# Performance work log

Hardware: AMD Instinct MI355X
Metric: run time of the kernel (lower is better)

## Reference

```python
import jax, jax.numpy as jnp
import numpy as np

INPUT_DIM = 256
UNITS = 256
BATCH = 65536


def _glorot(key, shape):
    fan_in, fan_out = shape
    limit = np.sqrt(6.0 / (fan_in + fan_out)).astype(np.float32)
    return jax.random.uniform(key, shape, jnp.float32, -limit, limit)


def setup_inputs() -> dict:
    key = jax.random.key(0)
    ks = jax.random.split(key, 8)
    d = {
        "inputs": jax.random.normal(ks[0], (BATCH, INPUT_DIM), jnp.float32),
        "h_prev": jax.random.normal(ks[1], (BATCH, UNITS), jnp.float32),
        "c_prev": jax.random.normal(ks[2], (BATCH, UNITS), jnp.float32),
        "W_f": _glorot(ks[3], (INPUT_DIM + UNITS, UNITS)),
        "W_i": _glorot(ks[4], (INPUT_DIM + UNITS, UNITS)),
        "W_c": _glorot(ks[5], (INPUT_DIM + UNITS, UNITS)),
        "W_o": _glorot(ks[6], (INPUT_DIM + UNITS, UNITS)),
        "b_f": jnp.zeros((UNITS,), jnp.float32),
        "b_i": jnp.zeros((UNITS,), jnp.float32),
        "b_c": jnp.zeros((UNITS,), jnp.float32),
        "b_o": jnp.zeros((UNITS,), jnp.float32),
    }
    return d


def reference(inputs, h_prev, c_prev, W_f, W_i, W_c, W_o, b_f, b_i, b_c, b_o):
    # z: [B, input_dim + units]
    z = jnp.concatenate([inputs, h_prev], axis=-1)
    f = jax.nn.sigmoid(z @ W_f + b_f)
    i = jax.nn.sigmoid(z @ W_i + b_i)
    c_tilde = jnp.tanh(z @ W_c + b_c)
    c = f * c_prev + i * c_tilde
    o = jax.nn.sigmoid(z @ W_o + b_o)
    h = o * jnp.tanh(c)
    return h, c
```

## Files before the change

### kernel.cpp

```cpp
#include <hip/hip_runtime.h>
#include <hip/hip_bf16.h>
#include <stdint.h>

#define BATCH   65536
#define UNITS   256
#define NCH     16
#define ROWP    68
#define GSZ     (64 * ROWP)
#define SMEM_BYTES 40960

using f32x16 = __attribute__((ext_vector_type(16))) float;
using bf16x8 = __attribute__((ext_vector_type(8))) short;

__device__ __forceinline__ short f2bf(float f) {
  union { float f; unsigned u; } v; v.f = f;
  unsigned r = v.u + 0x7FFFu + ((v.u >> 16) & 1u);
  return (short)(r >> 16);
}
__device__ __forceinline__ float bf2f(short s) {
  union { float f; unsigned u; } v; v.u = ((unsigned)(unsigned short)s) << 16;
  return v.f;
}
__device__ __forceinline__ unsigned pk2(float a, float b) {
  union { __hip_bfloat162 h; unsigned u; } cv;
  cv.h = __float22bfloat162_rn(make_float2(a, b));
  return cv.u;
}
__device__ __forceinline__ bf16x8 cvt8(float4 a, float4 b) {
  union { unsigned u[4]; bf16x8 v; } r;
  r.u[0] = pk2(a.x, a.y); r.u[1] = pk2(a.z, a.w);
  r.u[2] = pk2(b.x, b.y); r.u[3] = pk2(b.z, b.w);
  return r.v;
}
#define LOG2E 1.4426950408889634f
__device__ __forceinline__ float fast_sigmoid(float x) {
  return __builtin_amdgcn_rcpf(1.f + __builtin_amdgcn_exp2f(x * -LOG2E));
}
__device__ __forceinline__ float fast_tanh(float x) {
  return 2.f * __builtin_amdgcn_rcpf(1.f + __builtin_amdgcn_exp2f(x * (-2.f * LOG2E))) - 1.f;
}

#define BAR() do { asm volatile("s_waitcnt lgkmcnt(0)" ::: "memory"); \
                   __builtin_amdgcn_s_barrier(); } while (0)
#define WAITV(n) asm volatile("s_waitcnt vmcnt(" #n ")" ::: "memory")

__device__ __forceinline__ void gload_lds16(const void* gsrc, void* ldst) {
  __builtin_amdgcn_global_load_lds(
      (const __attribute__((address_space(1))) void*)gsrc,
      (__attribute__((address_space(3))) void*)ldst,
      16, 0, 0);
}

__global__ void cvt_weights(const float* __restrict__ Wf, const float* __restrict__ Wi,
                            const float* __restrict__ Wc, const float* __restrict__ Wo,
                            short* __restrict__ Wt) {
  int idx = blockIdx.x * 256 + threadIdx.x;
  int g   = idx >> 17;
  int k   = (idx >> 8) & 511;
  int col = idx & 255;
  const float* W = (g == 0) ? Wf : (g == 1) ? Wi : (g == 2) ? Wc : Wo;
  float val = W[k * 256 + col];
  int nb = col >> 6, n = col & 63;
  int kg = k >> 3, k8 = k & 7;
  int out = (((g * 4 + nb) * 64 + kg) * 64 + n) * 8 + k8;
  Wt[out] = f2bf(val);
}

__global__ __launch_bounds__(256, 4) void lstm_fused(
    const float* __restrict__ x, const float* __restrict__ hprev,
    const float* __restrict__ cprev, const short* __restrict__ Wt,
    const float* __restrict__ bfp, const float* __restrict__ bip,
    const float* __restrict__ bcp, const float* __restrict__ bop,
    float* __restrict__ hout, float* __restrict__ cout)
{
  extern __shared__ __align__(16) char smem[];
  const int tid  = threadIdx.x;
  const int g    = tid >> 6;
  const int lane = tid & 63;
  const int la   = lane & 31;
  const int hh   = lane >> 5;

  int bid = blockIdx.x;
  int wg  = (bid & 7) * 512 + (bid >> 3);
  const int m0 = (wg >> 2) * 64;
  const int nb = wg & 3;
  const int n0 = nb * 64;

  const short* WtG = Wt + ((size_t)(g * 4 + nb)) * 32768;

  f32x16 acc[2][2] = {};
  float4 vA[2][2];

  const int arow  = tid >> 2;
  const int q     = tid & 3;
  const int slotW = arow ^ (q << 2);

  char* Abase = smem;
  char* Bbase = smem + 8192;

  auto ldA = [&](int c) {
    const float* base = (c < 8) ? x : hprev;
    const float* rowp = base + (size_t)(m0 + arow) * 256 + (c & 7) * 32 + q * 8;
    vA[c & 1][0] = *(const float4*)(rowp);
    vA[c & 1][1] = *(const float4*)(rowp + 4);
  };
  auto wrA = [&](int c) {
    char* Ab = Abase + (c & 1) * 4096;
    *(bf16x8*)(Ab + q * 1024 + slotW * 16) = cvt8(vA[c & 1][0], vA[c & 1][1]);
  };
  auto stageB = [&](int c) {
    char* ldst = Bbase + (c & 1) * 16384 + g * 4096;
    const short* gs = WtG + c * 2048 + lane * 8;
#pragma unroll
    for (int i = 0; i < 4; ++i)
      gload_lds16(gs + i * 512, ldst + i * 1024);
  };
  auto compute = [&](int c) {
    const char* Ab = Abase + (c & 1) * 4096;
    const char* Bl = Bbase + (c & 1) * 16384 + g * 4096;
#pragma unroll
    for (int ks = 0; ks < 2; ++ks) {
      const int kg = 2 * ks + hh;
      const int ao = kg * 1024 + ((la ^ (kg << 2)) * 16);
      bf16x8 a0 = *(const bf16x8*)(Ab + ao);
      bf16x8 a1 = *(const bf16x8*)(Ab + ao + 512);
      bf16x8 b0 = *(const bf16x8*)(Bl + kg * 1024 + la * 16);
      bf16x8 b1 = *(const bf16x8*)(Bl + kg * 1024 + la * 16 + 512);
      acc[0][0] = __builtin_amdgcn_mfma_f32_32x32x16_bf16(a0, b0, acc[0][0], 0, 0, 0);
      acc[0][1] = __builtin_amdgcn_mfma_f32_32x32x16_bf16(a0, b1, acc[0][1], 0, 0, 0);
      acc[1][0] = __builtin_amdgcn_mfma_f32_32x32x16_bf16(a1, b0, acc[1][0], 0, 0, 0);
      acc[1][1] = __builtin_amdgcn_mfma_f32_32x32x16_bf16(a1, b1, acc[1][1], 0, 0, 0);
    }
  };

  ldA(0); stageB(0); ldA(1); stageB(1);
  wrA(0);

#pragma unroll
  for (int c = 0; c < NCH; ++c) {
    if (c + 2 < NCH) ldA(c + 2);
    if (c < NCH - 2)      WAITV(8);
    else if (c == NCH - 2) WAITV(6);
    else                   WAITV(0);
    BAR();
    if (c + 1 < NCH) wrA(c + 1);
    compute(c);
    __builtin_amdgcn_sched_barrier(0);
    if (c + 2 < NCH) stageB(c + 2);
  }

  const int ccol = tid & 63;
  const int rg   = tid >> 6;
  const size_t gbase = (size_t)(m0 + rg * 16) * 256 + n0 + ccol;
  float cp[16];
#pragma unroll
  for (int j = 0; j < 16; ++j) cp[j] = cprev[gbase + (size_t)j * 256];

  const float* bptr = (g == 0) ? bfp : (g == 1) ? bip : (g == 2) ? bcp : bop;
  const float bias0 = bptr[n0 + la];
  const float bias1 = bptr[n0 + 32 + la];
  BAR();
  short* G = (short*)smem;
#pragma unroll
  for (int mi = 0; mi < 2; ++mi)
#pragma unroll
    for (int ni = 0; ni < 2; ++ni) {
      const float bias = ni ? bias1 : bias0;
      const int   col  = la + ni * 32;
#pragma unroll
      for (int rq = 0; rq < 4; ++rq) {
        const int row0 = rq * 8 + 4 * hh + mi * 32;
        float t[4];
#pragma unroll
        for (int e = 0; e < 4; ++e) {
          float vv = acc[mi][ni][rq * 4 + e] + bias;
          t[e] = (g == 2) ? fast_tanh(vv) : fast_sigmoid(vv);
        }
        uint2 u; u.x = pk2(t[0], t[1]); u.y = pk2(t[2], t[3]);
        *(uint2*)(G + g * GSZ + col * ROWP + row0) = u;
      }
    }
  BAR();

  {
    const short* Gp = G + ccol * ROWP + rg * 16;
    bf16x8 gf[4][2];
#pragma unroll
    for (int gg = 0; gg < 4; ++gg) {
      gf[gg][0] = *(const bf16x8*)(Gp + gg * GSZ);
      gf[gg][1] = *(const bf16x8*)(Gp + gg * GSZ + 8);
    }
#pragma unroll
    for (int j = 0; j < 16; ++j) {
      float fg = bf2f(gf[0][j >> 3][j & 7]);
      float ig = bf2f(gf[1][j >> 3][j & 7]);
      float cg = bf2f(gf[2][j >> 3][j & 7]);
      float og = bf2f(gf[3][j >> 3][j & 7]);
      float cnew = fg * cp[j] + ig * cg;
      float hnew = og * fast_tanh(cnew);
      hout[gbase + (size_t)j * 256] = hnew;
      cout[gbase + (size_t)j * 256] = cnew;
    }
  }
}

extern "C" void kernel_launch(void* const* d_in, const int* in_sizes, int n_in,
                              void* d_out, int out_size, void* d_ws, size_t ws_size,
                              hipStream_t stream) {
  const float* x     = (const float*)d_in[0];
  const float* hprev = (const float*)d_in[1];
  const float* cprev = (const float*)d_in[2];
  const float* Wf    = (const float*)d_in[3];
  const float* Wi    = (const float*)d_in[4];
  const float* Wc    = (const float*)d_in[5];
  const float* Wo    = (const float*)d_in[6];
  const float* bfp   = (const float*)d_in[7];
  const float* bip   = (const float*)d_in[8];
  const float* bcp   = (const float*)d_in[9];
  const float* bop   = (const float*)d_in[10];
  float* out = (float*)d_out;
  short* Wt  = (short*)d_ws;

  cvt_weights<<<2048, 256, 0, stream>>>(Wf, Wi, Wc, Wo, Wt);

  lstm_fused<<<dim3(4096), dim3(256), SMEM_BYTES, stream>>>(
      x, hprev, cprev, Wt, bfp, bip, bcp, bop,
      out, out + (size_t)BATCH * UNITS);
}
```

Baseline: 143.5 us.

## Double block M tile to 128 rows with 512 threads sharing B stages

Each block now handles 128 batch rows using 512 threads (two M halves), so each weight chunk staged into LDS is reused by twice as many rows and global weight traffic is halved. The B buffer becomes triple-buffered, and the A global loads move after compute so they issue next to the B staging, with simplified vmcnt waits. The epilogue writes and combines the gate tiles in two phases through the same LDS region. The cost is more LDS per block (64KB), which may cut resident blocks per CU, plus extra barriers in the epilogue.

```diff
diff --git a/kernel.cpp b/kernel.cpp
--- a/kernel.cpp
+++ b/kernel.cpp
@@ -7,7 +7,7 @@
 #define NCH     16
 #define ROWP    68
 #define GSZ     (64 * ROWP)
-#define SMEM_BYTES 40960
+#define SMEM_BYTES 65536
 
 using f32x16 = __attribute__((ext_vector_type(16))) float;
 using bf16x8 = __attribute__((ext_vector_type(8))) short;
@@ -66,7 +66,7 @@
   Wt[out] = f2bf(val);
 }
 
-__global__ __launch_bounds__(256, 4) void lstm_fused(
+__global__ __launch_bounds__(512, 4) void lstm_fused(
     const float* __restrict__ x, const float* __restrict__ hprev,
     const float* __restrict__ cprev, const short* __restrict__ Wt,
     const float* __restrict__ bfp, const float* __restrict__ bip,
@@ -75,28 +75,28 @@
 {
   extern __shared__ __align__(16) char smem[];
   const int tid  = threadIdx.x;
-  const int g    = tid >> 6;
+  const int gg   = (tid >> 6) & 3;
+  const int mh   = tid >> 8;
   const int lane = tid & 63;
   const int la   = lane & 31;
   const int hh   = lane >> 5;
 
   int bid = blockIdx.x;
-  int wg  = (bid & 7) * 512 + (bid >> 3);
-  const int m0 = (wg >> 2) * 64;
+  int wg  = (bid & 7) * 256 + (bid >> 3);
+  const int m0 = (wg >> 2) * 128;
   const int nb = wg & 3;
   const int n0 = nb * 64;
 
-  const short* WtG = Wt + ((size_t)(g * 4 + nb)) * 32768;
+  const short* WtG = Wt + ((size_t)(gg * 4 + nb)) * 32768;
 
   f32x16 acc[2][2] = {};
   float4 vA[2][2];
 
-  const int arow  = tid >> 2;
-  const int q     = tid & 3;
-  const int slotW = arow ^ (q << 2);
+  const int arow = tid >> 2;
+  const int q    = tid & 3;
 
   char* Abase = smem;
-  char* Bbase = smem + 8192;
+  char* Bbase = smem + 16384;
 
   auto ldA = [&](int c) {
     const float* base = (c < 8) ? x : hprev;
@@ -105,23 +105,22 @@
     vA[c & 1][1] = *(const float4*)(rowp + 4);
   };
   auto wrA = [&](int c) {
-    char* Ab = Abase + (c & 1) * 4096;
-    *(bf16x8*)(Ab + q * 1024 + slotW * 16) = cvt8(vA[c & 1][0], vA[c & 1][1]);
+    char* Ab = Abase + (c & 1) * 8192;
+    *(bf16x8*)(Ab + q * 2048 + (arow ^ (q << 2)) * 16) = cvt8(vA[c & 1][0], vA[c & 1][1]);
   };
   auto stageB = [&](int c) {
-    char* ldst = Bbase + (c & 1) * 16384 + g * 4096;
-    const short* gs = WtG + c * 2048 + lane * 8;
-#pragma unroll
-    for (int i = 0; i < 4; ++i)
-      gload_lds16(gs + i * 512, ldst + i * 1024);
+    char* ldst = Bbase + (c % 3) * 16384 + gg * 4096 + mh * 2048;
+    const short* gs = WtG + c * 2048 + mh * 1024 + lane * 8;
+    gload_lds16(gs, ldst);
+    gload_lds16(gs + 512, ldst + 1024);
   };
   auto compute = [&](int c) {
-    const char* Ab = Abase + (c & 1) * 4096;
-    const char* Bl = Bbase + (c & 1) * 16384 + g * 4096;
+    const char* Ab = Abase + (c & 1) * 8192;
+    const char* Bl = Bbase + (c % 3) * 16384 + gg * 4096;
 #pragma unroll
     for (int ks = 0; ks < 2; ++ks) {
       const int kg = 2 * ks + hh;
-      const int ao = kg * 1024 + ((la ^ (kg << 2)) * 16);
+      const int ao = kg * 2048 + (((mh * 64 + la) ^ (kg << 2)) * 16);
       bf16x8 a0 = *(const bf16x8*)(Ab + ao);
       bf16x8 a1 = *(const bf16x8*)(Ab + ao + 512);
       bf16x8 b0 = *(const bf16x8*)(Bl + kg * 1024 + la * 16);
@@ -138,70 +137,77 @@
 
 #pragma unroll
   for (int c = 0; c < NCH; ++c) {
-    if (c + 2 < NCH) ldA(c + 2);
-    if (c < NCH - 2)      WAITV(8);
-    else if (c == NCH - 2) WAITV(6);
-    else                   WAITV(0);
+    if (c == NCH - 1) { WAITV(0); } else { WAITV(4); }
     BAR();
     if (c + 1 < NCH) wrA(c + 1);
     compute(c);
     __builtin_amdgcn_sched_barrier(0);
-    if (c + 2 < NCH) stageB(c + 2);
+    if (c + 2 < NCH) { ldA(c + 2); stageB(c + 2); }
   }
 
   const int ccol = tid & 63;
-  const int rg   = tid >> 6;
-  const size_t gbase = (size_t)(m0 + rg * 16) * 256 + n0 + ccol;
+  const int rseg = (tid >> 6) & 7;
   float cp[16];
 #pragma unroll
-  for (int j = 0; j < 16; ++j) cp[j] = cprev[gbase + (size_t)j * 256];
-
-  const float* bptr = (g == 0) ? bfp : (g == 1) ? bip : (g == 2) ? bcp : bop;
+  for (int ph = 0; ph < 2; ++ph) {
+    const size_t gb = (size_t)(m0 + ph * 64 + rseg * 8) * 256 + n0 + ccol;
+#pragma unroll
+    for (int j = 0; j < 8; ++j) cp[ph * 8 + j] = cprev[gb + (size_t)j * 256];
+  }
+
+  const float* bptr = (gg == 0) ? bfp : (gg == 1) ? bip : (gg == 2) ? bcp : bop;
   const float bias0 = bptr[n0 + la];
   const float bias1 = bptr[n0 + 32 + la];
-  BAR();
   short* G = (short*)smem;
-#pragma unroll
-  for (int mi = 0; mi < 2; ++mi)
-#pragma unroll
-    for (int ni = 0; ni < 2; ++ni) {
-      const float bias = ni ? bias1 : bias0;
-      const int   col  = la + ni * 32;
-#pragma unroll
-      for (int rq = 0; rq < 4; ++rq) {
-        const int row0 = rq * 8 + 4 * hh + mi * 32;
-        float t[4];
-#pragma unroll
-        for (int e = 0; e < 4; ++e) {
-          float vv = acc[mi][ni][rq * 4 + e] + bias;
-          t[e] = (g == 2) ? fast_tanh(vv) : fast_sigmoid(vv);
+
+  auto writeG = [&]() {
+#pragma unroll
+    for (int mi = 0; mi < 2; ++mi)
+#pragma unroll
+      for (int ni = 0; ni < 2; ++ni) {
+        const float bias = ni ? bias1 : bias0;
+        const int   col  = la + ni * 32;
+#pragma unroll
+        for (int rq = 0; rq < 4; ++rq) {
+          const int row0 = rq * 8 + 4 * hh + mi * 32;
+          float t[4];
+#pragma unroll
+          for (int e = 0; e < 4; ++e) {
+            float vv = acc[mi][ni][rq * 4 + e] + bias;
+            t[e] = (gg == 2) ? fast_tanh(vv) : fast_sigmoid(vv);
+          }
+          uint2 u; u.x = pk2(t[0], t[1]); u.y = pk2(t[2], t[3]);
+          *(uint2*)(G + gg * GSZ + col * ROWP + row0) = u;
         }
-        uint2 u; u.x = pk2(t[0], t[1]); u.y = pk2(t[2], t[3]);
-        *(uint2*)(G + g * GSZ + col * ROWP + row0) = u;
       }
+  };
+  auto combine = [&](int ph) {
+    const short* Gp = G + ccol * ROWP + rseg * 8;
+    bf16x8 gf[4];
+#pragma unroll
+    for (int t = 0; t < 4; ++t) gf[t] = *(const bf16x8*)(Gp + t * GSZ);
+    const size_t gb = (size_t)(m0 + ph * 64 + rseg * 8) * 256 + n0 + ccol;
+#pragma unroll
+    for (int j = 0; j < 8; ++j) {
+      float fg = bf2f(gf[0][j]);
+      float ig = bf2f(gf[1][j]);
+      float cg = bf2f(gf[2][j]);
+      float og = bf2f(gf[3][j]);
+      float cnew = fg * cp[ph * 8 + j] + ig * cg;
+      float hnew = og * fast_tanh(cnew);
+      hout[gb + (size_t)j * 256] = hnew;
+      cout[gb + (size_t)j * 256] = cnew;
     }
-  BAR();
-
-  {
-    const short* Gp = G + ccol * ROWP + rg * 16;
-    bf16x8 gf[4][2];
-#pragma unroll
-    for (int gg = 0; gg < 4; ++gg) {
-      gf[gg][0] = *(const bf16x8*)(Gp + gg * GSZ);
-      gf[gg][1] = *(const bf16x8*)(Gp + gg * GSZ + 8);
-    }
-#pragma unroll
-    for (int j = 0; j < 16; ++j) {
-      float fg = bf2f(gf[0][j >> 3][j & 7]);
-      float ig = bf2f(gf[1][j >> 3][j & 7]);
-      float cg = bf2f(gf[2][j >> 3][j & 7]);
-      float og = bf2f(gf[3][j >> 3][j & 7]);
-      float cnew = fg * cp[j] + ig * cg;
-      float hnew = og * fast_tanh(cnew);
-      hout[gbase + (size_t)j * 256] = hnew;
-      cout[gbase + (size_t)j * 256] = cnew;
-    }
-  }
+  };
+
+  BAR();
+  if (mh == 0) writeG();
+  BAR();
+  combine(0);
+  BAR();
+  if (mh == 1) writeG();
+  BAR();
+  combine(1);
 }
 
 extern "C" void kernel_launch(void* const* d_in, const int* in_sizes, int n_in,
@@ -223,7 +229,7 @@
 
   cvt_weights<<<2048, 256, 0, stream>>>(Wf, Wi, Wc, Wo, Wt);
 
-  lstm_fused<<<dim3(4096), dim3(256), SMEM_BYTES, stream>>>(
+  lstm_fused<<<dim3(2048), dim3(512), SMEM_BYTES, stream>>>(
       x, hprev, cprev, Wt, bfp, bip, bcp, bop,
       out, out + (size_t)BATCH * UNITS);
 }
```

After: 151.3 us. 5.4% more time.
